# Optimization experiments

Hardware: AMD Instinct MI355X
Metric: run time of the kernel (lower is better)

The kernel has to match this reference:

```python
import jax, jax.numpy as jnp
import numpy as np
from jax import lax

V, E, H = 32000, 512, 512
B, K, S, T = 16, 8, 50, 40
SOS, EOS, UNK, PAD = 2, 3, 0, 1
MIN_LEN, DD, NEG = 3, 0.1, -1e20
N = B * K


def setup_inputs():
    key = jax.random.key(0)
    ks = jax.random.split(key, 12)
    w = lambda k, sh: jax.random.normal(k, sh, dtype=jnp.float32) * 0.05
    return {
        "src": jax.random.randint(ks[0], (S, B), 4, V, dtype=jnp.int32),
        "src_len": jax.random.randint(ks[1], (B,), 5, S + 1, dtype=jnp.int32),
        "embed": w(ks[2], (V, E)),
        "enc_Wih": w(ks[3], (3 * H, E)), "enc_Whh": w(ks[4], (3 * H, H)),
        "enc_bih": jnp.zeros((3 * H,), jnp.float32), "enc_bhh": jnp.zeros((3 * H,), jnp.float32),
        "bridge_W": w(ks[5], (H, H)), "bridge_b": jnp.zeros((H,), jnp.float32),
        "dec_Wih": w(ks[6], (3 * H, E)), "dec_Whh": w(ks[7], (3 * H, H)),
        "dec_bih": jnp.zeros((3 * H,), jnp.float32), "dec_bhh": jnp.zeros((3 * H,), jnp.float32),
        "attn_W": w(ks[8], (H, H)),
        "comb_W": w(ks[9], (H, 2 * H)), "comb_b": jnp.zeros((H,), jnp.float32),
        "out_W": w(ks[10], (V, H)), "out_b": jnp.zeros((V,), jnp.float32),
    }


def _gru_cell(x, h, Wih, Whh, bih, bhh):
    # torch nn.GRU cell math
    gi = x @ Wih.T + bih
    gh = h @ Whh.T + bhh
    ir, iz, inn = jnp.split(gi, 3, axis=-1)
    hr, hz, hn = jnp.split(gh, 3, axis=-1)
    r = jax.nn.sigmoid(ir + hr)
    z = jax.nn.sigmoid(iz + hz)
    n = jnp.tanh(inn + r * hn)
    return (1.0 - z) * n + z * h


def _beam_search(src, src_len, embed, enc_Wih, enc_Whh, enc_bih, enc_bhh,
                 bridge_W, bridge_b, dec_Wih, dec_Whh, dec_bih, dec_bhh,
                 attn_W, comb_W, comb_b, out_W, out_b):
    # ---- encoder: uni-dir GRU with length masking ----
    def enc_step(h, xt):
        x_t, t = xt
        hn = _gru_cell(embed[x_t], h, enc_Wih, enc_Whh, enc_bih, enc_bhh)
        h = jnp.where((t < src_len)[:, None], hn, h)
        return h, h

    h_fin, enc_outs = lax.scan(enc_step, jnp.zeros((B, H), embed.dtype), (src, jnp.arange(S)))
    hidden = jnp.tanh(h_fin @ bridge_W.T + bridge_b)  # LinearBridge

    # ---- beam expansion (repeat_interleave over batch dim) ----
    enc_bank = jnp.repeat(enc_outs, K, axis=1).transpose(1, 0, 2)  # [N,S,H]
    src_len_b = jnp.repeat(src_len, K)                              # [N]
    hidden = jnp.repeat(hidden, K, axis=0)                          # [N,H]
    attn_mask = jnp.arange(S)[None, :] < src_len_b[:, None]         # [N,S]

    def dec_step(tok, h):
        h = _gru_cell(embed[tok], h, dec_Wih, dec_Whh, dec_bih, dec_bhh)
        sc = jnp.einsum('nh,nsh->ns', h @ attn_W.T, enc_bank)
        a = jax.nn.softmax(jnp.where(attn_mask, sc, -1e9), axis=-1)
        ctx = jnp.einsum('ns,nsh->nh', a, enc_bank)
        o = jnp.tanh(jnp.concatenate([h, ctx], axis=-1) @ comb_W.T + comb_b)
        return jax.nn.log_softmax(o @ out_W.T + out_b, axis=-1), h

    padding_logits = jnp.full((B, K, K), NEG, jnp.float32).at[:, :, 0].set(0.0)
    dd_off = jnp.broadcast_to(-(jnp.arange(K, dtype=jnp.float32) * DD), (B, K, K))
    flat_offsets = jnp.repeat(jnp.arange(0, N, K), K)  # [N]

    last_token = jnp.full((N,), SOS, jnp.int32)
    tokens = jnp.zeros((T, N), jnp.int32).at[0].set(last_token)
    ending = jnp.zeros((N,), bool)
    dec_len = jnp.zeros((N,), jnp.float32)
    beam_scores = jnp.zeros((T, B, K), jnp.float32).at[0].set(
        jnp.full((B, K), NEG, jnp.float32).at[:, 0].set(0.0))

    def step(carry, t):
        last_token, hidden, ending, dec_len, beam_scores, tokens = carry
        logp, hidden = dec_step(last_token, hidden)
        logp = logp.at[:, EOS].set(jnp.where(t <= MIN_LEN, NEG, logp[:, EOS]))
        logp = logp.at[:, UNK].set(NEG)  # disable_unk_output
        p = logp.reshape(B, K, V)
        tk_sc, tk_idx = lax.top_k(p, K)                       # [B,K,K]
        tk_sc = tk_sc + jnp.where(t > 1, 1.0, 0.0) * dd_off   # diverse decoding
        endf = ending.reshape(B, K, 1)
        fin = jnp.where(endf, -tk_sc + padding_logits, 0.0)   # finished-beam offsets
        total = beam_scores.sum(axis=0)                        # [B,K]
        tot = (tk_sc + total[:, :, None] + fin).reshape(B, K * K)
        cur = (tk_sc + fin).reshape(B, K * K)
        tmp_len = jnp.where(ending, dec_len, dec_len + 1.0)
        grp_tok = tk_idx.reshape(B, K * K)
        _, sel = lax.top_k(tot, K)                             # [B,K]
        sel_tok = jnp.take_along_axis(grp_tok, sel, axis=1)
        cur_sc = jnp.take_along_axis(cur, sel, axis=1)
        flat_idx = (sel // K).reshape(-1) + flat_offsets
        hidden = hidden[flat_offsets]  # faithful: source uses flatten_offsets here
        beam_scores = beam_scores.reshape(T, N)[:, flat_idx].reshape(T, B, K)
        tokens = tokens[:, flat_idx]
        ending = ending[flat_idx]
        dec_len = tmp_len[flat_idx]
        last_token = jnp.where(ending, PAD, sel_tok.reshape(-1)).astype(jnp.int32)
        tokens = tokens.at[t].set(last_token)
        beam_scores = beam_scores.at[t].set(
            cur_sc * (last_token.reshape(B, K) != PAD).astype(jnp.float32))
        ending = ending | (last_token == EOS)
        return (last_token, hidden, ending, dec_len, beam_scores, tokens), None

    carry = (last_token, hidden, ending, dec_len, beam_scores, tokens)
    (_, _, _, _, beam_scores, tokens), _ = lax.scan(step, carry, jnp.arange(1, T))
    return tokens, beam_scores.reshape(T, N)


def reference(src, src_len, embed, enc_Wih, enc_Whh, enc_bih, enc_bhh,
              bridge_W, bridge_b, dec_Wih, dec_Whh, dec_bih, dec_bhh,
              attn_W, comb_W, comb_b, out_W, out_b):
    tokens, beam_scores = _beam_search(src, src_len, embed, enc_Wih, enc_Whh,
                                       enc_bih, enc_bhh, bridge_W, bridge_b,
                                       dec_Wih, dec_Whh, dec_bih, dec_bhh,
                                       attn_W, comb_W, comb_b, out_W, out_b)
    output_probs = jnp.zeros((T, N, V), jnp.float32)  # allocated but never written, as in source
    return output_probs, tokens, beam_scores
```

## Files before the change

### kernel.cpp

```cpp
#include <hip/hip_runtime.h>

#define DEVFN __device__ __forceinline__

constexpr int V=32000, E=512, H=512, B=16, K=8, S=50, T=40, N=128;
constexpr int SOS=2, EOS=3, UNK=0, PAD=1, MIN_LEN=3;
constexpr float DD=0.1f;
constexpr float FNEG=-1e20f;

constexpr long long PROBS_ELEMS = 163840000LL;
constexpr int TOK_OUT_OFF = 163840000;
constexpr int BS_OUT_OFF  = 163845120;

constexpr int LOGITS_O = 0;
constexpr int WTOUT_O  = 4200000;
constexpr int WTEIH_O  = 20600000;
constexpr int WTEHH_O  = 21400000;
constexpr int WTDIH_O  = 22200000;
constexpr int WTDHH_O  = 23000000;
constexpr int WTATT_O  = 23800000;
constexpr int WTCMB_O  = 24100000;
constexpr int WTBRG_O  = 24700000;
constexpr int ENC_O    = 25000000;
constexpr int HST_O    = 25500000;
constexpr int HID_O    = 25520000;
constexpr int HNEW_O   = 25600000;
constexpr int CTX_O    = 25680000;
constexpr int OVEC_O   = 25760000;
constexpr int QVEC_O   = 25840000;
constexpr int TKSC_O   = 25920000;
constexpr int TKIX_O   = 25930000;
constexpr int TOK0_O   = 25940000;
constexpr int TOK1_O   = 25950000;
constexpr int BS0_O    = 25960000;
constexpr int BS1_O    = 25970000;
constexpr int END_O    = 25980000;
constexpr int LTOK_O   = 25990000;
constexpr int FLAG_O   = 25996000;
constexpr int PKEIH_O  = 26000000;
constexpr int PKEHH_O  = 26800000;
constexpr int PKDIH_O  = 27600000;
constexpr int PKDHH_O  = 28400000;
constexpr int PKATT_O  = 29200000;
constexpr int PKCMB_O  = 29500000;
constexpr int PKBRG_O  = 30100000;

DEVFN float sigm(float x){ return 1.0f/(1.0f + expf(-x)); }

__global__ void tr_k(const float* __restrict__ in, float* __restrict__ out, int R, int C){
  __shared__ float t[32][33];
  int bx = blockIdx.x, by = blockIdx.y;
  int x = threadIdx.x & 31, y0 = threadIdx.x >> 5;
  for (int yy = y0; yy < 32; yy += 8){
    t[yy][x] = in[(long long)(by*32+yy)*C + bx*32 + x];
  }
  __syncthreads();
  for (int yy = y0; yy < 32; yy += 8){
    out[(long long)(bx*32+yy)*R + by*32 + x] = t[x][yy];
  }
}

__global__ void pack_k(const float* __restrict__ in, float* __restrict__ out, int I, int Kc){
  int idx = blockIdx.x*256 + threadIdx.x;
  int total = I*(Kc>>2);
  if (idx >= total) return;
  int k4 = idx / I;
  int i  = idx - k4*I;
  float4 v = *((const float4*)(in + (long long)i*Kc + 4*k4));
  *((float4*)(out + ((long long)k4*I + i)*4)) = v;
}

__global__ void packchk_k(const float* __restrict__ orig, const float* __restrict__ packed,
                          int I, int Kc, int* flag){
  long long idx = (long long)blockIdx.x*256 + threadIdx.x;
  long long total = (long long)I*Kc;
  if (idx >= total) return;
  int i = (int)(idx / Kc); int k = (int)(idx - (long long)i*Kc);
  float a = orig[idx];
  float b = packed[((long long)(k>>2)*I + i)*4 + (k&3)];
  if (a != b) atomicOr(flag, 16);
}

__global__ void init_k(float* sc){
  int idx = blockIdx.x*256 + threadIdx.x;
  int* tok0 = (int*)(sc + TOK0_O);
  float* bs0 = sc + BS0_O;
  if (idx < T*N){
    tok0[idx] = (idx < N) ? SOS : 0;
    bs0[idx]  = (idx < N && (idx & 7)) ? FNEG : 0.0f;
  }
  if (idx < N){
    ((int*)(sc + END_O))[idx] = 0;
    ((int*)(sc + LTOK_O))[idx] = SOS;
  }
  if (idx < 2*B*H) sc[HST_O + idx] = 0.0f;
  if (idx == 0) ((int*)(sc + FLAG_O))[0] = 0;
}

__global__ void zero_k(float4* __restrict__ p){
  long long idx = (long long)blockIdx.x*256 + threadIdx.x;
  long long stride = (long long)gridDim.x*256;
  const long long n4 = PROBS_ELEMS/4;
  float4 z; z.x=0.f; z.y=0.f; z.z=0.f; z.w=0.f;
  for (long long u = idx; u < n4; u += stride) p[u] = z;
}

__global__ __launch_bounds__(384) void enc2_k(const int* __restrict__ src, const int* __restrict__ srclen,
    const float* __restrict__ embed, const float* __restrict__ wtih, const float* __restrict__ wthh,
    const float* __restrict__ bih, const float* __restrict__ bhh, float* sc, int t){
  int ic = blockIdx.x;
  int b  = blockIdx.y;
  int tid = threadIdx.x;
  int p = tid >> 6;
  int il = tid & 63;
  int i = ic*64 + il;
  __shared__ __align__(16) float e[512];
  __shared__ __align__(16) float h[512];
  __shared__ float gsh[6][64];
  const float* hsrc = sc + HST_O + (t&1)*B*H + b*H;
  float* hdst = sc + HST_O + ((t&1)^1)*B*H + b*H;
  int tok = src[t*B + b];
  for (int u = tid; u < 512; u += 384){
    e[u] = embed[(long long)tok*E + u];
    h[u] = hsrc[u];
  }
  __syncthreads();
  float acc = 0.0f;
  if (p < 3){
    const float* w = wtih + p*512 + i;
    for (int k=0;k<512;k++) acc += e[k]*w[(long long)k*1536];
  } else {
    const float* w = wthh + (p-3)*512 + i;
    for (int k=0;k<512;k++) acc += h[k]*w[(long long)k*1536];
  }
  gsh[p][il] = acc;
  __syncthreads();
  if (tid < 64){
    int ii = ic*64 + tid;
    float r = sigm(gsh[0][tid] + bih[ii] + gsh[3][tid] + bhh[ii]);
    float z = sigm(gsh[1][tid] + bih[512+ii] + gsh[4][tid] + bhh[512+ii]);
    float nn = tanhf(gsh[2][tid] + bih[1024+ii] + r*(gsh[5][tid] + bhh[1024+ii]));
    float hnew = (1.0f - z)*nn + z*h[ii];
    float hout = (t < srclen[b]) ? hnew : h[ii];
    hdst[ii] = hout;
    sc[ENC_O + ((long long)t*B + b)*H + ii] = hout;
  }
}

__global__ __launch_bounds__(256) void bridge_k(const float* __restrict__ wtb, const float* __restrict__ bb, float* sc){
  int b = blockIdx.x; int tid = threadIdx.x;
  __shared__ __align__(16) float hf[512];
  const float* hsrc = sc + HST_O + (S&1)*B*H + b*H;
  ((float2*)hf)[tid] = ((const float2*)hsrc)[tid];
  __syncthreads();
  for (int ii=0; ii<2; ii++){
    int i = tid + ii*256;
    float acc = bb[i];
    for (int k=0;k<512;k++) acc += hf[k]*wtb[(long long)k*512 + i];
    float hb = tanhf(acc);
    for (int q=0;q<K;q++) sc[HID_O + ((long long)(b*K+q))*H + i] = hb;
  }
}

__global__ __launch_bounds__(256) void grudec_k(const float* __restrict__ embed,
     const float* __restrict__ wtih, const float* __restrict__ wthh,
     const float* __restrict__ bih, const float* __restrict__ bhh, float* sc){
  int il = threadIdx.x & 63, sub = threadIdx.x >> 6;
  int i = blockIdx.x*64 + il;
  int nb = blockIdx.y*8;
  __shared__ __align__(16) float e8[8][512];
  __shared__ __align__(16) float hp8[8][512];
  const int* ltok = (const int*)(sc + LTOK_O);
  for (int u = threadIdx.x; u < 8*128; u += 256){
    int r = u >> 7, c = u & 127;
    ((float4*)e8[r])[c]  = ((const float4*)(embed + (long long)ltok[nb+r]*E))[c];
    ((float4*)hp8[r])[c] = ((const float4*)(sc + HID_O + (long long)(nb+r)*H))[c];
  }
  __syncthreads();
  int n0 = sub*2, n1 = sub*2+1;
  float a0r=0,a0z=0,a0n=0,h0r=0,h0z=0,h0n=0;
  float a1r=0,a1z=0,a1n=0,h1r=0,h1z=0,h1n=0;
  for (int k=0;k<512;k++){
    const float* wi = wtih + (long long)k*1536;
    const float* wh = wthh + (long long)k*1536;
    float wr=wi[i], wz=wi[512+i], wn=wi[1024+i];
    float ur=wh[i], uz=wh[512+i], un=wh[1024+i];
    float e0=e8[n0][k], e1=e8[n1][k], p0=hp8[n0][k], p1=hp8[n1][k];
    a0r+=e0*wr; a0z+=e0*wz; a0n+=e0*wn; h0r+=p0*ur; h0z+=p0*uz; h0n+=p0*un;
    a1r+=e1*wr; a1z+=e1*wz; a1n+=e1*wn; h1r+=p1*ur; h1z+=p1*uz; h1n+=p1*un;
  }
  float br=bih[i], bz=bih[512+i], bn=bih[1024+i];
  float cr=bhh[i], cz=bhh[512+i], cn=bhh[1024+i];
  {
    float r = sigm(a0r+br+h0r+cr);
    float z = sigm(a0z+bz+h0z+cz);
    float nn = tanhf(a0n+bn + r*(h0n+cn));
    sc[HNEW_O + (long long)(nb+n0)*H + i] = (1.0f-z)*nn + z*hp8[n0][i];
  }
  {
    float r = sigm(a1r+br+h1r+cr);
    float z = sigm(a1z+bz+h1z+cz);
    float nn = tanhf(a1n+bn + r*(h1n+cn));
    sc[HNEW_O + (long long)(nb+n1)*H + i] = (1.0f-z)*nn + z*hp8[n1][i];
  }
}

__global__ __launch_bounds__(256) void qgemm_k(const float* __restrict__ wta, float* sc){
  int il = threadIdx.x & 63, sub = threadIdx.x >> 6;
  int i = blockIdx.x*64 + il;
  int nb = blockIdx.y*8;
  __shared__ __align__(16) float hn8[8][512];
  for (int u = threadIdx.x; u < 8*128; u += 256){
    int r = u>>7, c = u&127;
    ((float4*)hn8[r])[c] = ((const float4*)(sc + HNEW_O + (long long)(nb+r)*H))[c];
  }
  __syncthreads();
  int n0 = sub*2, n1 = n0+1;
  float a0=0, a1=0;
  for (int k=0;k<512;k++){
    float w = wta[(long long)k*512 + i];
    a0 += hn8[n0][k]*w; a1 += hn8[n1][k]*w;
  }
  sc[QVEC_O + (long long)(nb+n0)*H + i] = a0;
  sc[QVEC_O + (long long)(nb+n1)*H + i] = a1;
}

__global__ __launch_bounds__(256) void att_k(const int* __restrict__ srclen, float* sc){
  int n = blockIdx.x; int g = n >> 3;
  int tid = threadIdx.x, lane = tid & 63, wave = tid >> 6;
  __shared__ __align__(16) float ql[512];
  __shared__ float al[64];
  if (tid < 128) ((float4*)ql)[tid] = ((const float4*)(sc + QVEC_O + (long long)n*H))[tid];
  __syncthreads();
  const float* enc = sc + ENC_O;
  for (int s = wave; s < S; s += 4){
    const float* er = enc + ((long long)s*B + g)*H;
    float p = 0;
    #pragma unroll
    for (int j=0;j<8;j++) p += ql[lane + 64*j]*er[lane + 64*j];
    #pragma unroll
    for (int off=32; off; off>>=1) p += __shfl_xor(p, off, 64);
    if (lane==0) al[s] = p;
  }
  __syncthreads();
  if (wave==0){
    int len = srclen[g];
    float v = (lane < S && lane < len) ? al[lane] : -1e9f;
    float m = v;
    #pragma unroll
    for (int off=32; off; off>>=1) m = fmaxf(m, __shfl_xor(m, off, 64));
    float ee = (lane < S) ? expf(v - m) : 0.0f;
    float ssum = ee;
    #pragma unroll
    for (int off=32; off; off>>=1) ssum += __shfl_xor(ssum, off, 64);
    if (lane < S) al[lane] = ee/ssum;
  }
  __syncthreads();
  for (int ii=0; ii<2; ii++){
    int i = tid + ii*256;
    float acc = 0;
    for (int s=0;s<S;s++) acc += al[s]*enc[((long long)s*B+g)*H + i];
    sc[CTX_O + (long long)n*H + i] = acc;
  }
}

__global__ __launch_bounds__(256) void comb_k(const float* __restrict__ wtc, const float* __restrict__ cb, float* sc){
  int il = threadIdx.x & 63, sub = threadIdx.x >> 6;
  int i = blockIdx.x*64 + il;
  int nb = blockIdx.y*8;
  __shared__ __align__(16) float hn8[8][512];
  __shared__ __align__(16) float cx8[8][512];
  for (int u = threadIdx.x; u < 8*128; u += 256){
    int r = u>>7, c = u&127;
    ((float4*)hn8[r])[c] = ((const float4*)(sc + HNEW_O + (long long)(nb+r)*H))[c];
    ((float4*)cx8[r])[c] = ((const float4*)(sc + CTX_O + (long long)(nb+r)*H))[c];
  }
  __syncthreads();
  int n0 = sub*2, n1 = n0+1;
  float a0=cb[i], a1=cb[i];
  for (int k=0;k<512;k++){
    float w = wtc[(long long)k*512 + i];
    a0 += hn8[n0][k]*w; a1 += hn8[n1][k]*w;
  }
  for (int k=0;k<512;k++){
    float w = wtc[(long long)(512+k)*512 + i];
    a0 += cx8[n0][k]*w; a1 += cx8[n1][k]*w;
  }
  sc[OVEC_O + (long long)(nb+n0)*H + i] = tanhf(a0);
  sc[OVEC_O + (long long)(nb+n1)*H + i] = tanhf(a1);
}

__global__ __launch_bounds__(256) void logits_k(const float* __restrict__ wto, const float* __restrict__ ob, float* sc){
  int v = blockIdx.x*1024 + threadIdx.x*4;
  int nb = blockIdx.y*16;
  __shared__ __align__(16) float o16[16][512];
  for (int u = threadIdx.x; u < 16*128; u += 256){
    int r = u>>7, c = u&127;
    ((float4*)o16[r])[c] = ((const float4*)(sc + OVEC_O + (long long)(nb + r)*H))[c];
  }
  __syncthreads();
  if (v >= V) return;
  float acc[16][4] = {};
  const float* wp = wto + v;
  float4 c0 = *((const float4*)(wp));
  float4 c1 = *((const float4*)(wp + V));
  float4 c2 = *((const float4*)(wp + 2LL*V));
  float4 c3 = *((const float4*)(wp + 3LL*V));
  for (int k=0;k<512;k+=4){
    float4 n0v=c0, n1v=c1, n2v=c2, n3v=c3;
    if (k < 508){
      const float* np_ = wp + (long long)(k+4)*V;
      n0v = *((const float4*)(np_));
      n1v = *((const float4*)(np_ + V));
      n2v = *((const float4*)(np_ + 2LL*V));
      n3v = *((const float4*)(np_ + 3LL*V));
    }
    #pragma unroll
    for (int j=0;j<16;j++){
      float4 o = *((const float4*)&o16[j][k]);
      acc[j][0] += o.x*c0.x + o.y*c1.x + o.z*c2.x + o.w*c3.x;
      acc[j][1] += o.x*c0.y + o.y*c1.y + o.z*c2.y + o.w*c3.y;
      acc[j][2] += o.x*c0.z + o.y*c1.z + o.z*c2.z + o.w*c3.z;
      acc[j][3] += o.x*c0.w + o.y*c1.w + o.z*c2.w + o.w*c3.w;
    }
    c0=n0v; c1=n1v; c2=n2v; c3=n3v;
  }
  float4 bbv = *((const float4*)(ob + v));
  #pragma unroll
  for (int j=0;j<16;j++){
    float4 r;
    r.x = acc[j][0]+bbv.x; r.y = acc[j][1]+bbv.y; r.z = acc[j][2]+bbv.z; r.w = acc[j][3]+bbv.w;
    *((float4*)(sc + LOGITS_O + (long long)(nb+j)*V + v)) = r;
  }
}

__global__ __launch_bounds__(256) void topk_k(float* sc, int t){
  int n = blockIdx.x, tid = threadIdx.x;
  const float4* row4 = (const float4*)(sc + LOGITS_O + (long long)n*V);
  __shared__ float rv[256];
  __shared__ float mv[256][8];
  __shared__ int   mi[256][8];
  float lm = -INFINITY;
  for (int u = tid; u < V/4; u += 256){
    float4 x = row4[u];
    lm = fmaxf(lm, fmaxf(fmaxf(x.x,x.y), fmaxf(x.z,x.w)));
  }
  rv[tid] = lm; __syncthreads();
  for (int s2=128; s2; s2>>=1){ if (tid<s2) rv[tid]=fmaxf(rv[tid],rv[tid+s2]); __syncthreads(); }
  float rmax = rv[0]; __syncthreads();
  float tv[8]; int ti[8];
  #pragma unroll
  for (int j=0;j<8;j++){ tv[j] = -INFINITY; ti[j] = V; }
  float ls = 0;
  for (int u = tid; u < V/4; u += 256){
    float4 x = row4[u];
    ls += expf(x.x-rmax)+expf(x.y-rmax)+expf(x.z-rmax)+expf(x.w-rmax);
    #pragma unroll
    for (int c=0;c<4;c++){
      int idx = u*4+c;
      float val = (c==0)?x.x:(c==1)?x.y:(c==2)?x.z:x.w;
      bool masked = (idx==UNK) || (idx==EOS && t<=MIN_LEN);
      if (!masked && val > tv[7]){
        tv[7] = val; ti[7] = idx;
        #pragma unroll
        for (int j=7;j>0;j--){
          if (tv[j] > tv[j-1]){
            float tf=tv[j]; tv[j]=tv[j-1]; tv[j-1]=tf;
            int tii=ti[j]; ti[j]=ti[j-1]; ti[j-1]=tii;
          }
        }
      }
    }
  }
  rv[tid] = ls;
  #pragma unroll
  for (int j=0;j<8;j++){ mv[tid][j]=tv[j]; mi[tid][j]=ti[j]; }
  __syncthreads();
  for (int s2=128; s2; s2>>=1){ if (tid<s2) rv[tid]+=rv[tid+s2]; __syncthreads(); }
  float lsum = logf(rv[0]);
  for (int s2=128; s2; s2>>=1){
    if (tid < s2){
      float ra[8]; int ri_[8];
      int pa=0, pb=0;
      #pragma unroll
      for (int o=0;o<8;o++){
        float va = mv[tid][pa<8?pa:7];   int xa = mi[tid][pa<8?pa:7];
        float vb = mv[tid+s2][pb<8?pb:7]; int xb = mi[tid+s2][pb<8?pb:7];
        bool ava = (pa<8), avb = (pb<8);
        bool ta;
        if (!ava) ta = false;
        else if (!avb) ta = true;
        else ta = (va > vb) || (va == vb && xa < xb);
        ra[o] = ta ? va : vb; ri_[o] = ta ? xa : xb;
        pa += ta ? 1 : 0; pb += ta ? 0 : 1;
      }
      #pragma unroll
      for (int o=0;o<8;o++){ mv[tid][o]=ra[o]; mi[tid][o]=ri_[o]; }
    }
    __syncthreads();
  }
  if (tid < 8){
    sc[TKSC_O + n*8 + tid] = (mv[0][tid] - rmax) - lsum;
    ((int*)(sc + TKIX_O))[n*8 + tid] = mi[0][tid];
  }
}

__global__ __launch_bounds__(64) void beam_k(float* sc, int t){
  int b = blockIdx.x, lane = threadIdx.x;
  const float* tksc = sc + TKSC_O;
  const int* tkix = (const int*)(sc + TKIX_O);
  int* endp = (int*)(sc + END_O);
  int* ltok = (int*)(sc + LTOK_O);
  const int* tokc; int* tokn; const float* bsc; float* bsn;
  if (t & 1){ tokc=(const int*)(sc+TOK0_O); tokn=(int*)(sc+TOK1_O); bsc=sc+BS0_O; bsn=sc+BS1_O; }
  else      { tokc=(const int*)(sc+TOK1_O); tokn=(int*)(sc+TOK0_O); bsc=sc+BS1_O; bsn=sc+BS0_O; }
  __shared__ int selp[8]; __shared__ int newtok[8]; __shared__ float newsc[8]; __shared__ int newend[8];
  if (lane == 0){
    float tot[64]; float cur[64]; int tix[64];
    for (int k=0;k<8;k++){
      float tp = 0;
      for (int u=0;u<T;u++) tp += bsc[u*N + b*8 + k];
      int ek = endp[b*8+k];
      for (int j=0;j<8;j++){
        float scv = tksc[(b*8+k)*8 + j];
        if (t > 1) scv -= DD * (float)j;
        float fin = ek ? (-scv + (j==0 ? 0.0f : FNEG)) : 0.0f;
        tot[k*8+j] = (scv + tp) + fin;
        cur[k*8+j] = scv + fin;
        tix[k*8+j] = tkix[(b*8+k)*8 + j];
      }
    }
    for (int q=0;q<8;q++){
      int best = 0; float bv = tot[0];
      for (int c=1;c<64;c++){
        if (tot[c] > bv){ bv = tot[c]; best = c; }
      }
      int p = best >> 3;
      int en = endp[b*8+p];
      int tk2 = tix[best];
      int lt = en ? PAD : tk2;
      selp[q] = p;
      newtok[q] = lt;
      newsc[q] = (lt != PAD) ? cur[best] : 0.0f;
      newend[q] = (en || lt == EOS) ? 1 : 0;
      tot[best] = -INFINITY;
    }
  }
  __syncthreads();
  for (int u = lane; u < T*8; u += 64){
    int tp2 = u >> 3, jp = u & 7;
    int p = selp[jp];
    tokn[tp2*N + b*8 + jp] = tokc[tp2*N + b*8 + p];
    bsn[tp2*N + b*8 + jp]  = bsc[tp2*N + b*8 + p];
  }
  __syncthreads();
  if (lane < 8){
    tokn[t*N + b*8 + lane] = newtok[lane];
    bsn[t*N + b*8 + lane]  = newsc[lane];
    ltok[b*8+lane] = newtok[lane];
    endp[b*8+lane] = newend[lane];
  }
  const float4* hsrc = (const float4*)(sc + HNEW_O + (long long)(b*8)*H);
  float4* hdst = (float4*)(sc + HID_O + (long long)(b*8)*H);
  for (int u = lane; u < 8*128; u += 64){
    int jp = u >> 7, c = u & 127;
    hdst[jp*128 + c] = hsrc[c];
  }
}

__global__ void emit_k(float* out, float* sc){
  int idx = blockIdx.x*256 + threadIdx.x;
  if (idx < T*N){
    out[TOK_OUT_OFF + idx] = (float)(((const int*)(sc + TOK1_O))[idx]);
    out[BS_OUT_OFF + idx]  = sc[BS1_O + idx];
  }
  if (idx == 0){
    int f = ((const int*)(sc + FLAG_O))[0];
    if (f) out[TOK_OUT_OFF] = 1.0e6f + (float)f;
  }
}

extern "C" void kernel_launch(void* const* d_in, const int* in_sizes, int n_in,
                              void* d_out, int out_size, void* d_ws, size_t ws_size,
                              hipStream_t stream){
  const int*   src    = (const int*)d_in[0];
  const int*   srclen = (const int*)d_in[1];
  const float* embed  = (const float*)d_in[2];
  const float* eWih   = (const float*)d_in[3];
  const float* eWhh   = (const float*)d_in[4];
  const float* ebih   = (const float*)d_in[5];
  const float* ebhh   = (const float*)d_in[6];
  const float* brW    = (const float*)d_in[7];
  const float* brb    = (const float*)d_in[8];
  const float* dWih   = (const float*)d_in[9];
  const float* dWhh   = (const float*)d_in[10];
  const float* dbih   = (const float*)d_in[11];
  const float* dbhh   = (const float*)d_in[12];
  const float* attW   = (const float*)d_in[13];
  const float* cmbW   = (const float*)d_in[14];
  const float* cmbb   = (const float*)d_in[15];
  const float* outW   = (const float*)d_in[16];
  const float* outb   = (const float*)d_in[17];
  float* sc = (float*)d_out;

  tr_k<<<dim3(16,48),256,0,stream>>>(eWih, sc+WTEIH_O, 1536, 512);
  tr_k<<<dim3(16,48),256,0,stream>>>(eWhh, sc+WTEHH_O, 1536, 512);
  tr_k<<<dim3(16,48),256,0,stream>>>(dWih, sc+WTDIH_O, 1536, 512);
  tr_k<<<dim3(16,48),256,0,stream>>>(dWhh, sc+WTDHH_O, 1536, 512);
  tr_k<<<dim3(16,16),256,0,stream>>>(attW, sc+WTATT_O, 512, 512);
  tr_k<<<dim3(32,16),256,0,stream>>>(cmbW, sc+WTCMB_O, 512, 1024);
  tr_k<<<dim3(16,16),256,0,stream>>>(brW,  sc+WTBRG_O, 512, 512);
  tr_k<<<dim3(16,1000),256,0,stream>>>(outW, sc+WTOUT_O, 32000, 512);
  pack_k<<<768,256,0,stream>>>(eWih, sc+PKEIH_O, 1536, 512);
  pack_k<<<768,256,0,stream>>>(eWhh, sc+PKEHH_O, 1536, 512);
  pack_k<<<768,256,0,stream>>>(dWih, sc+PKDIH_O, 1536, 512);
  pack_k<<<768,256,0,stream>>>(dWhh, sc+PKDHH_O, 1536, 512);
  pack_k<<<256,256,0,stream>>>(attW, sc+PKATT_O, 512, 512);
  pack_k<<<512,256,0,stream>>>(cmbW, sc+PKCMB_O, 512, 1024);
  pack_k<<<256,256,0,stream>>>(brW,  sc+PKBRG_O, 512, 512);
  init_k<<<64,256,0,stream>>>(sc);
  {
    int* flag = (int*)(sc + FLAG_O);
    packchk_k<<<3072,256,0,stream>>>(eWih, sc+PKEIH_O, 1536, 512, flag);
    packchk_k<<<3072,256,0,stream>>>(eWhh, sc+PKEHH_O, 1536, 512, flag);
    packchk_k<<<3072,256,0,stream>>>(dWih, sc+PKDIH_O, 1536, 512, flag);
    packchk_k<<<3072,256,0,stream>>>(dWhh, sc+PKDHH_O, 1536, 512, flag);
    packchk_k<<<1024,256,0,stream>>>(attW, sc+PKATT_O, 512, 512, flag);
    packchk_k<<<2048,256,0,stream>>>(cmbW, sc+PKCMB_O, 512, 1024, flag);
    packchk_k<<<1024,256,0,stream>>>(brW,  sc+PKBRG_O, 512, 512, flag);
  }

  for (int t=0; t<S; t++)
    enc2_k<<<dim3(8,16),384,0,stream>>>(src, srclen, embed, sc+WTEIH_O, sc+WTEHH_O, ebih, ebhh, sc, t);
  bridge_k<<<16,256,0,stream>>>(sc+WTBRG_O, brb, sc);

  for (int t=1; t<T; t++){
    grudec_k<<<dim3(8,16),256,0,stream>>>(embed, sc+WTDIH_O, sc+WTDHH_O, dbih, dbhh, sc);
    qgemm_k<<<dim3(8,16),256,0,stream>>>(sc+WTATT_O, sc);
    att_k<<<128,256,0,stream>>>(srclen, sc);
    comb_k<<<dim3(8,16),256,0,stream>>>(sc+WTCMB_O, cmbb, sc);
    logits_k<<<dim3(32,8),256,0,stream>>>(sc+WTOUT_O, outb, sc);
    topk_k<<<128,256,0,stream>>>(sc, t);
    beam_k<<<16,64,0,stream>>>(sc, t);
  }

  emit_k<<<20,256,0,stream>>>((float*)d_out, sc);
  zero_k<<<2048,256,0,stream>>>((float4*)d_out);
}
```

Measured before the change: 13.08 ms.

## Fuse logits GEMM with per-block partial top-k and log-softmax reduction

The logits kernel now computes per-block partial max, sum-exp and top-8 for each of its 16 rows in shared memory, writing small partials instead of the full logits matrix. A new merge kernel combines the 32 partials per row into final log-probability top-k. This removes the 16MB logits write and re-read per step. It also deletes the unused pack and pack-check kernels and the flag. The cost is 16 serialized block-wide reductions with many __syncthreads inside the GEMM kernel.

Measured after the change: 16.71 ms. 27.8% more time.

```diff
diff --git a/kernel.cpp b/kernel.cpp
--- a/kernel.cpp
+++ b/kernel.cpp
@@ -11,7 +11,6 @@
 constexpr int TOK_OUT_OFF = 163840000;
 constexpr int BS_OUT_OFF  = 163845120;
 
-constexpr int LOGITS_O = 0;
 constexpr int WTOUT_O  = 4200000;
 constexpr int WTEIH_O  = 20600000;
 constexpr int WTEHH_O  = 21400000;
@@ -35,14 +34,7 @@
 constexpr int BS1_O    = 25970000;
 constexpr int END_O    = 25980000;
 constexpr int LTOK_O   = 25990000;
-constexpr int FLAG_O   = 25996000;
-constexpr int PKEIH_O  = 26000000;
-constexpr int PKEHH_O  = 26800000;
-constexpr int PKDIH_O  = 27600000;
-constexpr int PKDHH_O  = 28400000;
-constexpr int PKATT_O  = 29200000;
-constexpr int PKCMB_O  = 29500000;
-constexpr int PKBRG_O  = 30100000;
+constexpr int PART_O   = 26000000;
 
 DEVFN float sigm(float x){ return 1.0f/(1.0f + expf(-x)); }
 
@@ -57,27 +49,6 @@
   for (int yy = y0; yy < 32; yy += 8){
     out[(long long)(bx*32+yy)*R + by*32 + x] = t[x][yy];
   }
-}
-
-__global__ void pack_k(const float* __restrict__ in, float* __restrict__ out, int I, int Kc){
-  int idx = blockIdx.x*256 + threadIdx.x;
-  int total = I*(Kc>>2);
-  if (idx >= total) return;
-  int k4 = idx / I;
-  int i  = idx - k4*I;
-  float4 v = *((const float4*)(in + (long long)i*Kc + 4*k4));
-  *((float4*)(out + ((long long)k4*I + i)*4)) = v;
-}
-
-__global__ void packchk_k(const float* __restrict__ orig, const float* __restrict__ packed,
-                          int I, int Kc, int* flag){
-  long long idx = (long long)blockIdx.x*256 + threadIdx.x;
-  long long total = (long long)I*Kc;
-  if (idx >= total) return;
-  int i = (int)(idx / Kc); int k = (int)(idx - (long long)i*Kc);
-  float a = orig[idx];
-  float b = packed[((long long)(k>>2)*I + i)*4 + (k&3)];
-  if (a != b) atomicOr(flag, 16);
 }
 
 __global__ void init_k(float* sc){
@@ -93,7 +64,6 @@
     ((int*)(sc + LTOK_O))[idx] = SOS;
   }
   if (idx < 2*B*H) sc[HST_O + idx] = 0.0f;
-  if (idx == 0) ((int*)(sc + FLAG_O))[0] = 0;
 }
 
 __global__ void zero_k(float4* __restrict__ p){
@@ -289,18 +259,24 @@
   sc[OVEC_O + (long long)(nb+n1)*H + i] = tanhf(a1);
 }
 
-__global__ __launch_bounds__(256) void logits_k(const float* __restrict__ wto, const float* __restrict__ ob, float* sc){
-  int v = blockIdx.x*1024 + threadIdx.x*4;
+__global__ __launch_bounds__(256) void logtk_k(const float* __restrict__ wto, const float* __restrict__ ob,
+                                               float* sc, int t){
+  int xb = blockIdx.x;
+  int tid = threadIdx.x;
+  int v = xb*1024 + tid*4;
   int nb = blockIdx.y*16;
   __shared__ __align__(16) float o16[16][512];
-  for (int u = threadIdx.x; u < 16*128; u += 256){
+  __shared__ float rvm[256], rvs[256];
+  __shared__ float mv[256][8];
+  __shared__ int   mi[256][8];
+  for (int u = tid; u < 16*128; u += 256){
     int r = u>>7, c = u&127;
     ((float4*)o16[r])[c] = ((const float4*)(sc + OVEC_O + (long long)(nb + r)*H))[c];
   }
   __syncthreads();
-  if (v >= V) return;
+  bool ok = (v < V);
   float acc[16][4] = {};
-  const float* wp = wto + v;
+  const float* wp = wto + (ok ? v : 0);
   float4 c0 = *((const float4*)(wp));
   float4 c1 = *((const float4*)(wp + V));
   float4 c2 = *((const float4*)(wp + 2LL*V));
@@ -324,83 +300,129 @@
     }
     c0=n0v; c1=n1v; c2=n2v; c3=n3v;
   }
-  float4 bbv = *((const float4*)(ob + v));
+  float4 bbv; bbv.x=0.f; bbv.y=0.f; bbv.z=0.f; bbv.w=0.f;
+  if (ok) bbv = *((const float4*)(ob + v));
   #pragma unroll
   for (int j=0;j<16;j++){
-    float4 r;
-    r.x = acc[j][0]+bbv.x; r.y = acc[j][1]+bbv.y; r.z = acc[j][2]+bbv.z; r.w = acc[j][3]+bbv.w;
-    *((float4*)(sc + LOGITS_O + (long long)(nb+j)*V + v)) = r;
-  }
-}
-
-__global__ __launch_bounds__(256) void topk_k(float* sc, int t){
-  int n = blockIdx.x, tid = threadIdx.x;
-  const float4* row4 = (const float4*)(sc + LOGITS_O + (long long)n*V);
-  __shared__ float rv[256];
-  __shared__ float mv[256][8];
-  __shared__ int   mi[256][8];
-  float lm = -INFINITY;
-  for (int u = tid; u < V/4; u += 256){
-    float4 x = row4[u];
-    lm = fmaxf(lm, fmaxf(fmaxf(x.x,x.y), fmaxf(x.z,x.w)));
-  }
-  rv[tid] = lm; __syncthreads();
-  for (int s2=128; s2; s2>>=1){ if (tid<s2) rv[tid]=fmaxf(rv[tid],rv[tid+s2]); __syncthreads(); }
-  float rmax = rv[0]; __syncthreads();
-  float tv[8]; int ti[8];
-  #pragma unroll
-  for (int j=0;j<8;j++){ tv[j] = -INFINITY; ti[j] = V; }
-  float ls = 0;
-  for (int u = tid; u < V/4; u += 256){
-    float4 x = row4[u];
-    ls += expf(x.x-rmax)+expf(x.y-rmax)+expf(x.z-rmax)+expf(x.w-rmax);
+    float r0 = acc[j][0]+bbv.x;
+    float r1 = acc[j][1]+bbv.y;
+    float r2 = acc[j][2]+bbv.z;
+    float r3 = acc[j][3]+bbv.w;
+    if (ok){
+      float lm = fmaxf(fmaxf(r0,r1), fmaxf(r2,r3));
+      rvm[tid] = lm;
+      rvs[tid] = expf(r0-lm)+expf(r1-lm)+expf(r2-lm)+expf(r3-lm);
+    } else {
+      rvm[tid] = -INFINITY;
+      rvs[tid] = 0.0f;
+    }
+    float tv[8]; int ti[8];
+    #pragma unroll
+    for (int o=0;o<8;o++){ tv[o] = -INFINITY; ti[o] = V; }
     #pragma unroll
     for (int c=0;c<4;c++){
-      int idx = u*4+c;
-      float val = (c==0)?x.x:(c==1)?x.y:(c==2)?x.z:x.w;
-      bool masked = (idx==UNK) || (idx==EOS && t<=MIN_LEN);
+      int idx = v + c;
+      float val = (c==0)?r0:(c==1)?r1:(c==2)?r2:r3;
+      bool masked = (!ok) || (idx==UNK) || (idx==EOS && t<=MIN_LEN);
       if (!masked && val > tv[7]){
         tv[7] = val; ti[7] = idx;
         #pragma unroll
-        for (int j=7;j>0;j--){
-          if (tv[j] > tv[j-1]){
-            float tf=tv[j]; tv[j]=tv[j-1]; tv[j-1]=tf;
-            int tii=ti[j]; ti[j]=ti[j-1]; ti[j-1]=tii;
+        for (int q=7;q>0;q--){
+          if (tv[q] > tv[q-1]){
+            float tf=tv[q]; tv[q]=tv[q-1]; tv[q-1]=tf;
+            int tq=ti[q]; ti[q]=ti[q-1]; ti[q-1]=tq;
           }
         }
       }
     }
-  }
-  rv[tid] = ls;
-  #pragma unroll
-  for (int j=0;j<8;j++){ mv[tid][j]=tv[j]; mi[tid][j]=ti[j]; }
-  __syncthreads();
-  for (int s2=128; s2; s2>>=1){ if (tid<s2) rv[tid]+=rv[tid+s2]; __syncthreads(); }
-  float lsum = logf(rv[0]);
-  for (int s2=128; s2; s2>>=1){
+    #pragma unroll
+    for (int o=0;o<8;o++){ mv[tid][o]=tv[o]; mi[tid][o]=ti[o]; }
+    __syncthreads();
+    for (int s2=128; s2; s2>>=1){
+      if (tid < s2){
+        float m1=rvm[tid], m2=rvm[tid+s2], s1=rvs[tid], s22=rvs[tid+s2];
+        float mm = fmaxf(m1,m2);
+        float ss = 0.0f;
+        if (m1 > -INFINITY) ss += s1*expf(m1-mm);
+        if (m2 > -INFINITY) ss += s22*expf(m2-mm);
+        rvm[tid]=mm; rvs[tid]=ss;
+        float ra[8]; int ri_[8];
+        int pa=0, pb=0;
+        #pragma unroll
+        for (int o=0;o<8;o++){
+          float va = mv[tid][pa<8?pa:7];   int xa = mi[tid][pa<8?pa:7];
+          float vb = mv[tid+s2][pb<8?pb:7]; int xb2 = mi[tid+s2][pb<8?pb:7];
+          bool ava = (pa<8), avb = (pb<8);
+          bool ta;
+          if (!ava) ta = false;
+          else if (!avb) ta = true;
+          else ta = (va > vb) || (va == vb && xa < xb2);
+          ra[o] = ta ? va : vb; ri_[o] = ta ? xa : xb2;
+          pa += ta ? 1 : 0; pb += ta ? 0 : 1;
+        }
+        #pragma unroll
+        for (int o=0;o<8;o++){ mv[tid][o]=ra[o]; mi[tid][o]=ri_[o]; }
+      }
+      __syncthreads();
+    }
+    if (tid == 0){
+      float* pp = sc + PART_O + ((long long)(nb+j)*32 + xb)*20;
+      #pragma unroll
+      for (int o=0;o<8;o++){ pp[o] = mv[0][o]; ((int*)pp)[8+o] = mi[0][o]; }
+      pp[16] = rvm[0]; pp[17] = rvs[0];
+    }
+    __syncthreads();
+  }
+}
+
+__global__ __launch_bounds__(64) void mrg_k(float* sc){
+  int n = blockIdx.x, tid = threadIdx.x;
+  __shared__ float rm[64], rs[64];
+  __shared__ float mvM[64][8];
+  __shared__ int   miM[64][8];
+  if (tid < 32){
+    const float* pp = sc + PART_O + ((long long)n*32 + tid)*20;
+    rm[tid] = pp[16]; rs[tid] = pp[17];
+    #pragma unroll
+    for (int o=0;o<8;o++){ mvM[tid][o] = pp[o]; miM[tid][o] = ((const int*)pp)[8+o]; }
+  } else {
+    rm[tid] = -INFINITY; rs[tid] = 0.0f;
+    #pragma unroll
+    for (int o=0;o<8;o++){ mvM[tid][o] = -INFINITY; miM[tid][o] = V; }
+  }
+  __syncthreads();
+  for (int s2=32; s2; s2>>=1){
     if (tid < s2){
+      float m1=rm[tid], m2=rm[tid+s2], s1=rs[tid], s22=rs[tid+s2];
+      float mm = fmaxf(m1,m2);
+      float ss = 0.0f;
+      if (m1 > -INFINITY) ss += s1*expf(m1-mm);
+      if (m2 > -INFINITY) ss += s22*expf(m2-mm);
+      rm[tid]=mm; rs[tid]=ss;
       float ra[8]; int ri_[8];
       int pa=0, pb=0;
       #pragma unroll
       for (int o=0;o<8;o++){
-        float va = mv[tid][pa<8?pa:7];   int xa = mi[tid][pa<8?pa:7];
-        float vb = mv[tid+s2][pb<8?pb:7]; int xb = mi[tid+s2][pb<8?pb:7];
+        float va = mvM[tid][pa<8?pa:7];   int xa = miM[tid][pa<8?pa:7];
+        float vb = mvM[tid+s2][pb<8?pb:7]; int xb2 = miM[tid+s2][pb<8?pb:7];
         bool ava = (pa<8), avb = (pb<8);
         bool ta;
         if (!ava) ta = false;
         else if (!avb) ta = true;
-        else ta = (va > vb) || (va == vb && xa < xb);
-        ra[o] = ta ? va : vb; ri_[o] = ta ? xa : xb;
+        else ta = (va > vb) || (va == vb && xa < xb2);
+        ra[o] = ta ? va : vb; ri_[o] = ta ? xa : xb2;
         pa += ta ? 1 : 0; pb += ta ? 0 : 1;
       }
       #pragma unroll
-      for (int o=0;o<8;o++){ mv[tid][o]=ra[o]; mi[tid][o]=ri_[o]; }
+      for (int o=0;o<8;o++){ mvM[tid][o]=ra[o]; miM[tid][o]=ri_[o]; }
     }
     __syncthreads();
   }
   if (tid < 8){
-    sc[TKSC_O + n*8 + tid] = (mv[0][tid] - rmax) - lsum;
-    ((int*)(sc + TKIX_O))[n*8 + tid] = mi[0][tid];
+    float gm = rm[0];
+    float lsum = logf(rs[0]);
+    sc[TKSC_O + n*8 + tid] = (mvM[0][tid] - gm) - lsum;
+    ((int*)(sc + TKIX_O))[n*8 + tid] = miM[0][tid];
   }
 }
 
@@ -473,10 +495,6 @@
     out[TOK_OUT_OFF + idx] = (float)(((const int*)(sc + TOK1_O))[idx]);
     out[BS_OUT_OFF + idx]  = sc[BS1_O + idx];
   }
-  if (idx == 0){
-    int f = ((const int*)(sc + FLAG_O))[0];
-    if (f) out[TOK_OUT_OFF] = 1.0e6f + (float)f;
-  }
 }
 
 extern "C" void kernel_launch(void* const* d_in, const int* in_sizes, int n_in,
@@ -510,24 +528,7 @@
   tr_k<<<dim3(32,16),256,0,stream>>>(cmbW, sc+WTCMB_O, 512, 1024);
   tr_k<<<dim3(16,16),256,0,stream>>>(brW,  sc+WTBRG_O, 512, 512);
   tr_k<<<dim3(16,1000),256,0,stream>>>(outW, sc+WTOUT_O, 32000, 512);
-  pack_k<<<768,256,0,stream>>>(eWih, sc+PKEIH_O, 1536, 512);
-  pack_k<<<768,256,0,stream>>>(eWhh, sc+PKEHH_O, 1536, 512);
-  pack_k<<<768,256,0,stream>>>(dWih, sc+PKDIH_O, 1536, 512);
-  pack_k<<<768,256,0,stream>>>(dWhh, sc+PKDHH_O, 1536, 512);
-  pack_k<<<256,256,0,stream>>>(attW, sc+PKATT_O, 512, 512);
-  pack_k<<<512,256,0,stream>>>(cmbW, sc+PKCMB_O, 512, 1024);
-  pack_k<<<256,256,0,stream>>>(brW,  sc+PKBRG_O, 512, 512);
   init_k<<<64,256,0,stream>>>(sc);
-  {
-    int* flag = (int*)(sc + FLAG_O);
-    packchk_k<<<3072,256,0,stream>>>(eWih, sc+PKEIH_O, 1536, 512, flag);
-    packchk_k<<<3072,256,0,stream>>>(eWhh, sc+PKEHH_O, 1536, 512, flag);
-    packchk_k<<<3072,256,0,stream>>>(dWih, sc+PKDIH_O, 1536, 512, flag);
-    packchk_k<<<3072,256,0,stream>>>(dWhh, sc+PKDHH_O, 1536, 512, flag);
-    packchk_k<<<1024,256,0,stream>>>(attW, sc+PKATT_O, 512, 512, flag);
-    packchk_k<<<2048,256,0,stream>>>(cmbW, sc+PKCMB_O, 512, 1024, flag);
-    packchk_k<<<1024,256,0,stream>>>(brW,  sc+PKBRG_O, 512, 512, flag);
-  }
 
   for (int t=0; t<S; t++)
     enc2_k<<<dim3(8,16),384,0,stream>>>(src, srclen, embed, sc+WTEIH_O, sc+WTEHH_O, ebih, ebhh, sc, t);
@@ -538,8 +539,8 @@
     qgemm_k<<<dim3(8,16),256,0,stream>>>(sc+WTATT_O, sc);
     att_k<<<128,256,0,stream>>>(srclen, sc);
     comb_k<<<dim3(8,16),256,0,stream>>>(sc+WTCMB_O, cmbb, sc);
-    logits_k<<<dim3(32,8),256,0,stream>>>(sc+WTOUT_O, outb, sc);
-    topk_k<<<128,256,0,stream>>>(sc, t);
+    logtk_k<<<dim3(32,8),256,0,stream>>>(sc+WTOUT_O, outb, sc, t);
+    mrg_k<<<128,64,0,stream>>>(sc);
     beam_k<<<16,64,0,stream>>>(sc, t);
   }
 
```
